# Performance work log

Measured on AMD Instinct MI355X. Metric: run time of the kernel, lower is better.

## Reference

```python
import jax, jax.numpy as jnp
import numpy as np

N_NODES = 100000

def gcn_layer(x, W, b, src, dst, norm):
    # x: [N, Fin], W: [Fin, Fout]; fused linear then normalized neighbor aggregation
    h = x @ W                                   # [N, Fout]
    msg = h[src] * norm[:, None]                # gather + per-edge scale, [E', Fout]
    agg = jax.ops.segment_sum(msg, dst, num_segments=N_NODES)  # scatter-add
    return agg + b

def _add_self_loops_and_norm(edge_index):
    src, dst = edge_index[0], edge_index[1]
    loop = jnp.arange(N_NODES, dtype=src.dtype)
    src = jnp.concatenate([src, loop])
    dst = jnp.concatenate([dst, loop])
    deg = jax.ops.segment_sum(jnp.ones_like(dst, dtype=jnp.float32), dst, num_segments=N_NODES)
    dis = jnp.where(deg > 0, jax.lax.rsqrt(deg), 0.0)   # deg^{-1/2}
    norm = dis[src] * dis[dst]                          # symmetric GCN normalization
    return src, dst, norm

def setup_inputs() -> dict:
    key = jax.random.key(0)
    k1, k2, k3, k4, k5, k6 = jax.random.split(key, 6)
    F_IN, F_HID, F_OUT = 64, 64, 64
    E = 1600000
    x = jax.random.normal(k1, (N_NODES, F_IN), dtype=jnp.float32)
    edge_index = jax.random.randint(k2, (2, E), 0, N_NODES, dtype=jnp.int64)
    s1 = 1.0 / np.sqrt(F_IN)
    s2 = 1.0 / np.sqrt(F_HID)
    W1 = jax.random.uniform(k3, (F_IN, F_HID), dtype=jnp.float32, minval=-s1, maxval=s1)
    b1 = jax.random.uniform(k4, (F_HID,), dtype=jnp.float32, minval=-s1, maxval=s1)
    W2 = jax.random.uniform(k5, (F_HID, F_OUT), dtype=jnp.float32, minval=-s2, maxval=s2)
    b2 = jax.random.uniform(k6, (F_OUT,), dtype=jnp.float32, minval=-s2, maxval=s2)
    return {"x": x, "edge_index": edge_index, "W1": W1, "b1": b1, "W2": W2, "b2": b2}

def reference(x, edge_index, W1, b1, W2, b2):
    src, dst, norm = _add_self_loops_and_norm(edge_index)
    h = gcn_layer(x, W1, b1, src, dst, norm)
    h = jax.nn.relu(h)
    h = gcn_layer(h, W2, b2, src, dst, norm)
    return h
```

## Files before the change

### kernel.cpp

```cpp
#include <hip/hip_runtime.h>
#include <cstdint>
#include <cstddef>


#define BK_SHIFT 9
#define BK_NODES 512
#define EPB 8192
#define CAP 12288
#define NBMAX 256

typedef short bf16x8 __attribute__((ext_vector_type(8)));
typedef float f32x4  __attribute__((ext_vector_type(4)));

static __device__ __forceinline__ unsigned short f2b(float f) {
    unsigned x = __float_as_uint(f);
    unsigned r = (x + 0x7FFFu + ((x >> 16) & 1u)) >> 16;
    return (unsigned short)r;
}
static __device__ __forceinline__ float blo(unsigned u) {
    return __uint_as_float(u << 16);
}
static __device__ __forceinline__ float bhi(unsigned u) {
    return __uint_as_float(u & 0xFFFF0000u);
}
static __device__ __forceinline__ void splitbf(float x, short& hi, short& lo) {
    unsigned short h = f2b(x);
    hi = (short)h;
    float r = x - __uint_as_float((unsigned)h << 16);
    lo = (short)f2b(r);
}

__global__ void k_init(int* __restrict__ gcursor, int NB) {
    int t = threadIdx.x;
    if (t < NB) gcursor[t] = t * CAP;
}

__global__ void __launch_bounds__(256) k_bscatter(const int* __restrict__ src,
                                                  const int* __restrict__ dst,
                                                  int* __restrict__ gcursor,
                                                  unsigned* __restrict__ packed,
                                                  int E, int NB) {
    __shared__ int hist[NBMAX];
    __shared__ int base[NBMAX];
    int t = threadIdx.x;
    for (int i = t; i < NB; i += 256) hist[i] = 0;
    __syncthreads();
    int e0 = blockIdx.x * EPB;
    int e1 = min(e0 + EPB, E);
    int4 dv[8];
    int kd[8];
#pragma unroll
    for (int k = 0; k < 8; ++k) {
        int e = e0 + t * 4 + k * 1024;
        kd[k] = (e + 3 < e1) ? 1 : 0;
        if (kd[k]) dv[k] = *(const int4*)(dst + e);
    }
#pragma unroll
    for (int k = 0; k < 8; ++k) {
        if (kd[k]) {
            atomicAdd(&hist[dv[k].x >> BK_SHIFT], 1);
            atomicAdd(&hist[dv[k].y >> BK_SHIFT], 1);
            atomicAdd(&hist[dv[k].z >> BK_SHIFT], 1);
            atomicAdd(&hist[dv[k].w >> BK_SHIFT], 1);
        }
    }
    __syncthreads();
    for (int i = t; i < NB; i += 256) {
        int c = hist[i];
        base[i] = c ? atomicAdd(&gcursor[i], c) : 0;
        hist[i] = 0;
    }
    __syncthreads();
    int4 sv[8];
#pragma unroll
    for (int k = 0; k < 8; ++k) {
        int e = e0 + t * 4 + k * 1024;
        if (kd[k]) sv[k] = *(const int4*)(src + e);
    }
#pragma unroll
    for (int k = 0; k < 8; ++k) {
        if (kd[k]) {
            int b0 = dv[k].x >> BK_SHIFT;
            int p0 = base[b0] + atomicAdd(&hist[b0], 1);
            packed[p0] = (unsigned)sv[k].x | (((unsigned)dv[k].x & (BK_NODES - 1)) << 17);
            int b1 = dv[k].y >> BK_SHIFT;
            int p1 = base[b1] + atomicAdd(&hist[b1], 1);
            packed[p1] = (unsigned)sv[k].y | (((unsigned)dv[k].y & (BK_NODES - 1)) << 17);
            int b2 = dv[k].z >> BK_SHIFT;
            int p2 = base[b2] + atomicAdd(&hist[b2], 1);
            packed[p2] = (unsigned)sv[k].z | (((unsigned)dv[k].z & (BK_NODES - 1)) << 17);
            int b3 = dv[k].w >> BK_SHIFT;
            int p3 = base[b3] + atomicAdd(&hist[b3], 1);
            packed[p3] = (unsigned)sv[k].w | (((unsigned)dv[k].w & (BK_NODES - 1)) << 17);
        }
    }
}

__global__ void __launch_bounds__(512) k_build(const unsigned* __restrict__ packed,
                                               const int* __restrict__ gcursor,
                                               int* __restrict__ rp,
                                               int* __restrict__ dega,
                                               float* __restrict__ dis,
                                               int* __restrict__ col, int N) {
    __shared__ int cnt_s[BK_NODES];
    __shared__ int tmp[BK_NODES];
    int b = blockIdx.x;
    int t = threadIdx.x;
    int node0 = b << BK_SHIFT;
    int nnode = min(BK_NODES, N - node0);
    int e0 = b * CAP;
    int e1 = gcursor[b];
    cnt_s[t] = 0;
    __syncthreads();
    for (int e = e0 + t * 4; e < e1; e += 2048) {
        int m = e1 - e; m = m > 4 ? 4 : m;
        unsigned p0 = packed[e];
        unsigned p1 = (m > 1) ? packed[e + 1] : 0;
        unsigned p2 = (m > 2) ? packed[e + 2] : 0;
        unsigned p3 = (m > 3) ? packed[e + 3] : 0;
        atomicAdd(&cnt_s[p0 >> 17], 1);
        if (m > 1) atomicAdd(&cnt_s[p1 >> 17], 1);
        if (m > 2) atomicAdd(&cnt_s[p2 >> 17], 1);
        if (m > 3) atomicAdd(&cnt_s[p3 >> 17], 1);
    }
    __syncthreads();
    int v = cnt_s[t];
    tmp[t] = v;
    __syncthreads();
    for (int off = 1; off < BK_NODES; off <<= 1) {
        int a = (t >= off) ? tmp[t - off] : 0;
        __syncthreads();
        tmp[t] += a;
        __syncthreads();
    }
    int excl = tmp[t] - v;
    if (t < nnode) {
        rp[node0 + t] = e0 + excl;
        dega[node0 + t] = v;
        dis[node0 + t] = rsqrtf((float)(v + 1));
    }
    __syncthreads();
    cnt_s[t] = excl;
    __syncthreads();
    for (int e = e0 + t * 4; e < e1; e += 2048) {
        int m = e1 - e; m = m > 4 ? 4 : m;
        unsigned p0 = packed[e];
        unsigned p1 = (m > 1) ? packed[e + 1] : 0;
        unsigned p2 = (m > 2) ? packed[e + 2] : 0;
        unsigned p3 = (m > 3) ? packed[e + 3] : 0;
        int pos0 = atomicAdd(&cnt_s[p0 >> 17], 1);
        col[e0 + pos0] = (int)(p0 & 0x1FFFFu);
        if (m > 1) { int pos = atomicAdd(&cnt_s[p1 >> 17], 1); col[e0 + pos] = (int)(p1 & 0x1FFFFu); }
        if (m > 2) { int pos = atomicAdd(&cnt_s[p2 >> 17], 1); col[e0 + pos] = (int)(p2 & 0x1FFFFu); }
        if (m > 3) { int pos = atomicAdd(&cnt_s[p3 >> 17], 1); col[e0 + pos] = (int)(p3 & 0x1FFFFu); }
    }
}

__global__ void __launch_bounds__(256) k_gemm_mfma(const float* __restrict__ X,
                                                   const float* __restrict__ W,
                                                   const float* __restrict__ dis,
                                                   unsigned short* __restrict__ g16,
                                                   int n, int nstrips) {
    __shared__ float Ws[4096];
    int t = threadIdx.x;
    {
        const float4* W4 = (const float4*)W;
        float4* S4 = (float4*)Ws;
#pragma unroll
        for (int i = 0; i < 4; ++i) S4[t + i * 256] = W4[t + i * 256];
    }
    __syncthreads();
    int wid  = t >> 6;
    int lane = t & 63;
    int quad = lane >> 4;
    int fl   = lane & 15;

    bf16x8 Bh[4][2], Bl[4][2];
#pragma unroll
    for (int tt = 0; tt < 4; ++tt)
#pragma unroll
        for (int c = 0; c < 2; ++c)
#pragma unroll
            for (int j = 0; j < 8; ++j) {
                float w = Ws[(c * 32 + quad * 8 + j) * 64 + tt * 16 + fl];
                short hi, lo;
                splitbf(w, hi, lo);
                Bh[tt][c][j] = hi;
                Bl[tt][c][j] = lo;
            }

    for (int s = blockIdx.x * 4 + wid; s < nstrips; s += gridDim.x * 4) {
        int row0 = s << 4;
        const float4* xp = (const float4*)(X + ((size_t)(row0 + fl) << 6));
        bf16x8 Ah[2], Al[2];
#pragma unroll
        for (int c = 0; c < 2; ++c) {
            float4 a = xp[c * 8 + quad * 2];
            float4 b = xp[c * 8 + quad * 2 + 1];
            float xs[8] = {a.x, a.y, a.z, a.w, b.x, b.y, b.z, b.w};
#pragma unroll
            for (int j = 0; j < 8; ++j) {
                short hi, lo;
                splitbf(xs[j], hi, lo);
                Ah[c][j] = hi;
                Al[c][j] = lo;
            }
        }
        f32x4 acc[4];
#pragma unroll
        for (int tt = 0; tt < 4; ++tt) acc[tt] = (f32x4){0.f, 0.f, 0.f, 0.f};
#pragma unroll
        for (int tt = 0; tt < 4; ++tt) {
#pragma unroll
            for (int c = 0; c < 2; ++c) {
                acc[tt] = __builtin_amdgcn_mfma_f32_16x16x32_bf16(Ah[c], Bh[tt][c], acc[tt], 0, 0, 0);
                acc[tt] = __builtin_amdgcn_mfma_f32_16x16x32_bf16(Al[c], Bh[tt][c], acc[tt], 0, 0, 0);
                acc[tt] = __builtin_amdgcn_mfma_f32_16x16x32_bf16(Ah[c], Bl[tt][c], acc[tt], 0, 0, 0);
            }
        }
        float4 dv = *(const float4*)(dis + row0 + quad * 4);
        float ds4[4] = {dv.x, dv.y, dv.z, dv.w};
#pragma unroll
        for (int tt = 0; tt < 4; ++tt) {
#pragma unroll
            for (int r = 0; r < 4; ++r) {
                int row = row0 + quad * 4 + r;
                float v = acc[tt][r] * ds4[r];
                g16[(size_t)row * 64 + tt * 16 + fl] = f2b(v);
            }
        }
    }
}

template <int RELU>
__global__ void __launch_bounds__(256) k_agg(const unsigned short* __restrict__ g16,
                                             const int* __restrict__ col,
                                             const int* __restrict__ rp,
                                             const int* __restrict__ dega,
                                             const float* __restrict__ dis,
                                             const float* __restrict__ bias,
                                             float* __restrict__ out, int n) {
    int lane = threadIdx.x & 63;
    int wv = (blockIdx.x << 2) | (threadIdx.x >> 6);
    int sub = lane >> 3;
    int fl  = lane & 7;
    int base = wv << 3;
    if (base >= n) return;
    int node = base + sub;
    int nd = min(node, n - 1);
    int start = rp[nd];
    int deg = (node < n) ? dega[nd] : 0;
    int dm = max(deg, __shfl_xor(deg, 8));
    dm = max(dm, __shfl_xor(dm, 16));
    dm = max(dm, __shfl_xor(dm, 32));

    uint4 us = *((const uint4*)(g16 + ((size_t)nd << 6)) + fl);
    float A[8], B[8], C[8], D[8];
    A[0] = blo(us.x); A[1] = bhi(us.x); A[2] = blo(us.y); A[3] = bhi(us.y);
    A[4] = blo(us.z); A[5] = bhi(us.z); A[6] = blo(us.w); A[7] = bhi(us.w);
#pragma unroll
    for (int j = 0; j < 8; ++j) { B[j] = 0.f; C[j] = 0.f; D[j] = 0.f; }

    int sb = sub << 3;
    for (int c = 0; c < dm; c += 8) {
        int rem = deg - c;
        int cv = 0;
        if (fl < rem) cv = col[start + c + fl];
        int rr[8];
#pragma unroll
        for (int i = 0; i < 8; ++i) rr[i] = __shfl(cv, sb + i);
        uint4 u[8];
#pragma unroll
        for (int i = 0; i < 8; ++i)
            if (i < rem) u[i] = *((const uint4*)(g16 + ((size_t)rr[i] << 6)) + fl);
#pragma unroll
        for (int i = 0; i < 8; ++i) {
            if (i < rem) {
                float* T = ((i & 3) == 0) ? A : ((i & 3) == 1) ? B : ((i & 3) == 2) ? C : D;
                T[0] += blo(u[i].x); T[1] += bhi(u[i].x);
                T[2] += blo(u[i].y); T[3] += bhi(u[i].y);
                T[4] += blo(u[i].z); T[5] += bhi(u[i].z);
                T[6] += blo(u[i].w); T[7] += bhi(u[i].w);
            }
        }
    }
    float s = dis[nd];
    float4 bv0 = ((const float4*)bias)[fl * 2];
    float4 bv1 = ((const float4*)bias)[fl * 2 + 1];
    float r[8];
#pragma unroll
    for (int j = 0; j < 8; ++j) r[j] = (A[j] + B[j]) + (C[j] + D[j]);
    float4 o0, o1;
    o0.x = fmaf(s, r[0], bv0.x); o0.y = fmaf(s, r[1], bv0.y);
    o0.z = fmaf(s, r[2], bv0.z); o0.w = fmaf(s, r[3], bv0.w);
    o1.x = fmaf(s, r[4], bv1.x); o1.y = fmaf(s, r[5], bv1.y);
    o1.z = fmaf(s, r[6], bv1.z); o1.w = fmaf(s, r[7], bv1.w);
    if (RELU) {
        o0.x = fmaxf(o0.x, 0.f); o0.y = fmaxf(o0.y, 0.f);
        o0.z = fmaxf(o0.z, 0.f); o0.w = fmaxf(o0.w, 0.f);
        o1.x = fmaxf(o1.x, 0.f); o1.y = fmaxf(o1.y, 0.f);
        o1.z = fmaxf(o1.z, 0.f); o1.w = fmaxf(o1.w, 0.f);
    }
    if (node < n) {
        float4* op = (float4*)(out + ((size_t)node << 6)) + fl * 2;
        op[0] = o0;
        op[1] = o1;
    }
}

extern "C" void kernel_launch(void* const* d_in, const int* in_sizes, int n_in,
                              void* d_out, int out_size, void* d_ws, size_t ws_size,
                              hipStream_t stream) {
    const float* x  = (const float*)d_in[0];
    const int*   ei = (const int*)d_in[1];
    const float* W1 = (const float*)d_in[2];
    const float* b1 = (const float*)d_in[3];
    const float* W2 = (const float*)d_in[4];
    const float* b2 = (const float*)d_in[5];
    float* out = (float*)d_out;

    const int N = in_sizes[0] / 64;
    const int E = in_sizes[1] / 2;
    const int NB = (N + BK_NODES - 1) >> BK_SHIFT;
    const int nstrips = (N + 15) >> 4;
    const int* src = ei;
    const int* dst = ei + E;

    char* ws = (char*)d_ws;
    size_t off = 0;
    auto alloc = [&](size_t bytes) -> void* {
        void* p = ws + off;
        off = (off + bytes + 255) & ~(size_t)255;
        return p;
    };
    int*            gcursor = (int*)alloc((size_t)NB * 4);
    int*            rp      = (int*)alloc((size_t)N * 4);
    int*            dega    = (int*)alloc((size_t)N * 4);
    float*          dis     = (float*)alloc((size_t)N * 4);
    unsigned*       packed  = (unsigned*)alloc((size_t)NB * CAP * 4);
    int*            col     = (int*)alloc((size_t)NB * CAP * 4);
    unsigned short* g16     = (unsigned short*)alloc((size_t)N * 64 * 2);
    float*          h       = (float*)alloc((size_t)N * 64 * 4);
    (void)ws_size;

    k_init<<<1, 256, 0, stream>>>(gcursor, NB);
    k_bscatter<<<(E + EPB - 1) / EPB, 256, 0, stream>>>(src, dst, gcursor, packed, E, NB);
    k_build<<<NB, 512, 0, stream>>>(packed, gcursor, rp, dega, dis, col, N);

    k_gemm_mfma<<<782, 256, 0, stream>>>(x, W1, dis, g16, N, nstrips);
    k_agg<1><<<(N + 31) / 32, 256, 0, stream>>>(g16, col, rp, dega, dis, b1, h, N);
    k_gemm_mfma<<<782, 256, 0, stream>>>(h, W2, dis, g16, N, nstrips);
    k_agg<0><<<(N + 31) / 32, 256, 0, stream>>>(g16, col, rp, dega, dis, b2, out, N);
}
```

Baseline: 206.7 us.

## Store hidden layer in bf16, retune scatter/build blocks, widen aggregation batch

The first aggregation now writes the ReLU'd hidden activations as bf16, and the second GEMM reads them directly. This halves that intermediate's traffic and drops the split-precision MFMA for the activation low part. The edge bucketing kernels use larger blocks with fewer edges per thread, and k_build runs 1024 threads. The aggregation loop gathers 16 neighbor rows per iteration instead of 8 for more memory-level parallelism. Rounding the hidden layer to bf16 loosens accuracy in the second layer.

Measured after the change: 207.4 us. About the same (+0.3%).

```diff
diff --git a/kernel.cpp b/kernel.cpp
--- a/kernel.cpp
+++ b/kernel.cpp
@@ -5,7 +5,7 @@
 
 #define BK_SHIFT 9
 #define BK_NODES 512
-#define EPB 8192
+#define EPB 4096
 #define CAP 12288
 #define NBMAX 256
 
@@ -35,7 +35,7 @@
     if (t < NB) gcursor[t] = t * CAP;
 }
 
-__global__ void __launch_bounds__(256) k_bscatter(const int* __restrict__ src,
+__global__ void __launch_bounds__(512) k_bscatter(const int* __restrict__ src,
                                                   const int* __restrict__ dst,
                                                   int* __restrict__ gcursor,
                                                   unsigned* __restrict__ packed,
@@ -43,20 +43,20 @@
     __shared__ int hist[NBMAX];
     __shared__ int base[NBMAX];
     int t = threadIdx.x;
-    for (int i = t; i < NB; i += 256) hist[i] = 0;
+    for (int i = t; i < NB; i += 512) hist[i] = 0;
     __syncthreads();
     int e0 = blockIdx.x * EPB;
     int e1 = min(e0 + EPB, E);
-    int4 dv[8];
-    int kd[8];
-#pragma unroll
-    for (int k = 0; k < 8; ++k) {
-        int e = e0 + t * 4 + k * 1024;
+    int4 dv[2];
+    int kd[2];
+#pragma unroll
+    for (int k = 0; k < 2; ++k) {
+        int e = e0 + t * 4 + k * 2048;
         kd[k] = (e + 3 < e1) ? 1 : 0;
         if (kd[k]) dv[k] = *(const int4*)(dst + e);
     }
 #pragma unroll
-    for (int k = 0; k < 8; ++k) {
+    for (int k = 0; k < 2; ++k) {
         if (kd[k]) {
             atomicAdd(&hist[dv[k].x >> BK_SHIFT], 1);
             atomicAdd(&hist[dv[k].y >> BK_SHIFT], 1);
@@ -65,20 +65,20 @@
         }
     }
     __syncthreads();
-    for (int i = t; i < NB; i += 256) {
+    for (int i = t; i < NB; i += 512) {
         int c = hist[i];
         base[i] = c ? atomicAdd(&gcursor[i], c) : 0;
         hist[i] = 0;
     }
     __syncthreads();
-    int4 sv[8];
-#pragma unroll
-    for (int k = 0; k < 8; ++k) {
-        int e = e0 + t * 4 + k * 1024;
+    int4 sv[2];
+#pragma unroll
+    for (int k = 0; k < 2; ++k) {
+        int e = e0 + t * 4 + k * 2048;
         if (kd[k]) sv[k] = *(const int4*)(src + e);
     }
 #pragma unroll
-    for (int k = 0; k < 8; ++k) {
+    for (int k = 0; k < 2; ++k) {
         if (kd[k]) {
             int b0 = dv[k].x >> BK_SHIFT;
             int p0 = base[b0] + atomicAdd(&hist[b0], 1);
@@ -96,12 +96,12 @@
     }
 }
 
-__global__ void __launch_bounds__(512) k_build(const unsigned* __restrict__ packed,
-                                               const int* __restrict__ gcursor,
-                                               int* __restrict__ rp,
-                                               int* __restrict__ dega,
-                                               float* __restrict__ dis,
-                                               int* __restrict__ col, int N) {
+__global__ void __launch_bounds__(1024) k_build(const unsigned* __restrict__ packed,
+                                                const int* __restrict__ gcursor,
+                                                int* __restrict__ rp,
+                                                int* __restrict__ dega,
+                                                float* __restrict__ dis,
+                                                int* __restrict__ col, int N) {
     __shared__ int cnt_s[BK_NODES];
     __shared__ int tmp[BK_NODES];
     int b = blockIdx.x;
@@ -110,9 +110,9 @@
     int nnode = min(BK_NODES, N - node0);
     int e0 = b * CAP;
     int e1 = gcursor[b];
-    cnt_s[t] = 0;
-    __syncthreads();
-    for (int e = e0 + t * 4; e < e1; e += 2048) {
+    if (t < BK_NODES) cnt_s[t] = 0;
+    __syncthreads();
+    for (int e = e0 + t * 4; e < e1; e += 4096) {
         int m = e1 - e; m = m > 4 ? 4 : m;
         unsigned p0 = packed[e];
         unsigned p1 = (m > 1) ? packed[e + 1] : 0;
@@ -124,25 +124,25 @@
         if (m > 3) atomicAdd(&cnt_s[p3 >> 17], 1);
     }
     __syncthreads();
-    int v = cnt_s[t];
-    tmp[t] = v;
+    int v = 0;
+    if (t < BK_NODES) { v = cnt_s[t]; tmp[t] = v; }
     __syncthreads();
     for (int off = 1; off < BK_NODES; off <<= 1) {
-        int a = (t >= off) ? tmp[t - off] : 0;
+        int a = (t < BK_NODES && t >= off) ? tmp[t - off] : 0;
         __syncthreads();
-        tmp[t] += a;
+        if (t < BK_NODES) tmp[t] += a;
         __syncthreads();
     }
-    int excl = tmp[t] - v;
     if (t < nnode) {
+        int excl = tmp[t] - v;
         rp[node0 + t] = e0 + excl;
         dega[node0 + t] = v;
         dis[node0 + t] = rsqrtf((float)(v + 1));
     }
     __syncthreads();
-    cnt_s[t] = excl;
-    __syncthreads();
-    for (int e = e0 + t * 4; e < e1; e += 2048) {
+    if (t < BK_NODES) cnt_s[t] = tmp[t] - v;
+    __syncthreads();
+    for (int e = e0 + t * 4; e < e1; e += 4096) {
         int m = e1 - e; m = m > 4 ? 4 : m;
         unsigned p0 = packed[e];
         unsigned p1 = (m > 1) ? packed[e + 1] : 0;
@@ -156,7 +156,9 @@
     }
 }
 
+template <int ABF16>
 __global__ void __launch_bounds__(256) k_gemm_mfma(const float* __restrict__ X,
+                                                   const unsigned short* __restrict__ X16,
                                                    const float* __restrict__ W,
                                                    const float* __restrict__ dis,
                                                    unsigned short* __restrict__ g16,
@@ -191,19 +193,25 @@
 
     for (int s = blockIdx.x * 4 + wid; s < nstrips; s += gridDim.x * 4) {
         int row0 = s << 4;
-        const float4* xp = (const float4*)(X + ((size_t)(row0 + fl) << 6));
         bf16x8 Ah[2], Al[2];
-#pragma unroll
-        for (int c = 0; c < 2; ++c) {
-            float4 a = xp[c * 8 + quad * 2];
-            float4 b = xp[c * 8 + quad * 2 + 1];
-            float xs[8] = {a.x, a.y, a.z, a.w, b.x, b.y, b.z, b.w};
-#pragma unroll
-            for (int j = 0; j < 8; ++j) {
-                short hi, lo;
-                splitbf(xs[j], hi, lo);
-                Ah[c][j] = hi;
-                Al[c][j] = lo;
+        if (ABF16) {
+            const bf16x8* hp = (const bf16x8*)(X16 + ((size_t)(row0 + fl) << 6));
+#pragma unroll
+            for (int c = 0; c < 2; ++c) Ah[c] = hp[c * 4 + quad];
+        } else {
+            const float4* xp = (const float4*)(X + ((size_t)(row0 + fl) << 6));
+#pragma unroll
+            for (int c = 0; c < 2; ++c) {
+                float4 a = xp[c * 8 + quad * 2];
+                float4 b = xp[c * 8 + quad * 2 + 1];
+                float xs[8] = {a.x, a.y, a.z, a.w, b.x, b.y, b.z, b.w};
+#pragma unroll
+                for (int j = 0; j < 8; ++j) {
+                    short hi, lo;
+                    splitbf(xs[j], hi, lo);
+                    Ah[c][j] = hi;
+                    Al[c][j] = lo;
+                }
             }
         }
         f32x4 acc[4];
@@ -214,8 +222,9 @@
 #pragma unroll
             for (int c = 0; c < 2; ++c) {
                 acc[tt] = __builtin_amdgcn_mfma_f32_16x16x32_bf16(Ah[c], Bh[tt][c], acc[tt], 0, 0, 0);
-                acc[tt] = __builtin_amdgcn_mfma_f32_16x16x32_bf16(Al[c], Bh[tt][c], acc[tt], 0, 0, 0);
                 acc[tt] = __builtin_amdgcn_mfma_f32_16x16x32_bf16(Ah[c], Bl[tt][c], acc[tt], 0, 0, 0);
+                if (!ABF16)
+                    acc[tt] = __builtin_amdgcn_mfma_f32_16x16x32_bf16(Al[c], Bh[tt][c], acc[tt], 0, 0, 0);
             }
         }
         float4 dv = *(const float4*)(dis + row0 + quad * 4);
@@ -232,14 +241,16 @@
     }
 }
 
-template <int RELU>
+template <int RELU, int OBF16>
 __global__ void __launch_bounds__(256) k_agg(const unsigned short* __restrict__ g16,
                                              const int* __restrict__ col,
                                              const int* __restrict__ rp,
                                              const int* __restrict__ dega,
                                              const float* __restrict__ dis,
                                              const float* __restrict__ bias,
-                                             float* __restrict__ out, int n) {
+                                             float* __restrict__ outf,
+                                             unsigned short* __restrict__ out16,
+                                             int n) {
     int lane = threadIdx.x & 63;
     int wv = (blockIdx.x << 2) | (threadIdx.x >> 6);
     int sub = lane >> 3;
@@ -262,19 +273,22 @@
     for (int j = 0; j < 8; ++j) { B[j] = 0.f; C[j] = 0.f; D[j] = 0.f; }
 
     int sb = sub << 3;
-    for (int c = 0; c < dm; c += 8) {
+    for (int c = 0; c < dm; c += 16) {
         int rem = deg - c;
-        int cv = 0;
-        if (fl < rem) cv = col[start + c + fl];
-        int rr[8];
-#pragma unroll
-        for (int i = 0; i < 8; ++i) rr[i] = __shfl(cv, sb + i);
-        uint4 u[8];
-#pragma unroll
-        for (int i = 0; i < 8; ++i)
+        int cv0 = 0, cv1 = 0;
+        if (fl < rem) cv0 = col[start + c + fl];
+        if (fl + 8 < rem) cv1 = col[start + c + 8 + fl];
+        int rr[16];
+#pragma unroll
+        for (int i = 0; i < 8; ++i) rr[i] = __shfl(cv0, sb + i);
+#pragma unroll
+        for (int i = 0; i < 8; ++i) rr[8 + i] = __shfl(cv1, sb + i);
+        uint4 u[16];
+#pragma unroll
+        for (int i = 0; i < 16; ++i)
             if (i < rem) u[i] = *((const uint4*)(g16 + ((size_t)rr[i] << 6)) + fl);
 #pragma unroll
-        for (int i = 0; i < 8; ++i) {
+        for (int i = 0; i < 16; ++i) {
             if (i < rem) {
                 float* T = ((i & 3) == 0) ? A : ((i & 3) == 1) ? B : ((i & 3) == 2) ? C : D;
                 T[0] += blo(u[i].x); T[1] += bhi(u[i].x);
@@ -290,21 +304,27 @@
     float r[8];
 #pragma unroll
     for (int j = 0; j < 8; ++j) r[j] = (A[j] + B[j]) + (C[j] + D[j]);
-    float4 o0, o1;
-    o0.x = fmaf(s, r[0], bv0.x); o0.y = fmaf(s, r[1], bv0.y);
-    o0.z = fmaf(s, r[2], bv0.z); o0.w = fmaf(s, r[3], bv0.w);
-    o1.x = fmaf(s, r[4], bv1.x); o1.y = fmaf(s, r[5], bv1.y);
-    o1.z = fmaf(s, r[6], bv1.z); o1.w = fmaf(s, r[7], bv1.w);
-    if (RELU) {
-        o0.x = fmaxf(o0.x, 0.f); o0.y = fmaxf(o0.y, 0.f);
-        o0.z = fmaxf(o0.z, 0.f); o0.w = fmaxf(o0.w, 0.f);
-        o1.x = fmaxf(o1.x, 0.f); o1.y = fmaxf(o1.y, 0.f);
-        o1.z = fmaxf(o1.z, 0.f); o1.w = fmaxf(o1.w, 0.f);
+    float bb[8] = {bv0.x, bv0.y, bv0.z, bv0.w, bv1.x, bv1.y, bv1.z, bv1.w};
+#pragma unroll
+    for (int j = 0; j < 8; ++j) {
+        r[j] = fmaf(s, r[j], bb[j]);
+        if (RELU) r[j] = fmaxf(r[j], 0.f);
     }
     if (node < n) {
-        float4* op = (float4*)(out + ((size_t)node << 6)) + fl * 2;
-        op[0] = o0;
-        op[1] = o1;
+        if (OBF16) {
+            uint4 pk;
+            pk.x = (unsigned)f2b(r[0]) | ((unsigned)f2b(r[1]) << 16);
+            pk.y = (unsigned)f2b(r[2]) | ((unsigned)f2b(r[3]) << 16);
+            pk.z = (unsigned)f2b(r[4]) | ((unsigned)f2b(r[5]) << 16);
+            pk.w = (unsigned)f2b(r[6]) | ((unsigned)f2b(r[7]) << 16);
+            *((uint4*)(out16 + ((size_t)node << 6)) + fl) = pk;
+        } else {
+            float4 o0 = {r[0], r[1], r[2], r[3]};
+            float4 o1 = {r[4], r[5], r[6], r[7]};
+            float4* op = (float4*)(outf + ((size_t)node << 6)) + fl * 2;
+            op[0] = o0;
+            op[1] = o1;
+        }
     }
 }
 
@@ -340,15 +360,15 @@
     unsigned*       packed  = (unsigned*)alloc((size_t)NB * CAP * 4);
     int*            col     = (int*)alloc((size_t)NB * CAP * 4);
     unsigned short* g16     = (unsigned short*)alloc((size_t)N * 64 * 2);
-    float*          h       = (float*)alloc((size_t)N * 64 * 4);
+    unsigned short* h16     = (unsigned short*)alloc((size_t)N * 64 * 2);
     (void)ws_size;
 
     k_init<<<1, 256, 0, stream>>>(gcursor, NB);
-    k_bscatter<<<(E + EPB - 1) / EPB, 256, 0, stream>>>(src, dst, gcursor, packed, E, NB);
-    k_build<<<NB, 512, 0, stream>>>(packed, gcursor, rp, dega, dis, col, N);
-
-    k_gemm_mfma<<<782, 256, 0, stream>>>(x, W1, dis, g16, N, nstrips);
-    k_agg<1><<<(N + 31) / 32, 256, 0, stream>>>(g16, col, rp, dega, dis, b1, h, N);
-    k_gemm_mfma<<<782, 256, 0, stream>>>(h, W2, dis, g16, N, nstrips);
-    k_agg<0><<<(N + 31) / 32, 256, 0, stream>>>(g16, col, rp, dega, dis, b2, out, N);
-}
+    k_bscatter<<<(E + EPB - 1) / EPB, 512, 0, stream>>>(src, dst, gcursor, packed, E, NB);
+    k_build<<<NB, 1024, 0, stream>>>(packed, gcursor, rp, dega, dis, col, N);
+
+    k_gemm_mfma<0><<<782, 256, 0, stream>>>(x, nullptr, W1, dis, g16, N, nstrips);
+    k_agg<1, 1><<<(N + 31) / 32, 256, 0, stream>>>(g16, col, rp, dega, dis, b1, nullptr, h16, N);
+    k_gemm_mfma<1><<<782, 256, 0, stream>>>(nullptr, h16, W2, dis, g16, N, nstrips);
+    k_agg<0, 0><<<(N + 31) / 32, 256, 0, stream>>>(g16, col, rp, dega, dis, b2, out, nullptr, N);
+}
```
